# Performance work log

Hardware: AMD Instinct MI355X
Metric: run time of the kernel (lower is better)

Reference implementation:

```python
import jax, jax.numpy as jnp
import numpy as np

H = 16
D_MODEL = 1024
D_K = D_MODEL // H
L = 4096


def setup_inputs() -> dict:
    key = jax.random.key(0)
    ks = jax.random.split(key, 11)
    s = 1.0 / np.sqrt(D_MODEL)
    inp = {
        "query": jax.random.normal(ks[0], (L, D_MODEL), dtype=jnp.float32),
        "key": jax.random.normal(ks[1], (L, D_MODEL), dtype=jnp.float32),
        "value": jax.random.normal(ks[2], (L, D_MODEL), dtype=jnp.float32),
        "Wq": jax.random.uniform(ks[3], (D_MODEL, D_MODEL), jnp.float32, -s, s),
        "Wk": jax.random.uniform(ks[4], (D_MODEL, D_MODEL), jnp.float32, -s, s),
        "Wv": jax.random.uniform(ks[5], (D_MODEL, D_MODEL), jnp.float32, -s, s),
        "Wo": jax.random.uniform(ks[6], (D_MODEL, D_MODEL), jnp.float32, -s, s),
        "bq": jax.random.uniform(ks[7], (D_MODEL,), jnp.float32, -s, s),
        "bk": jax.random.uniform(ks[8], (D_MODEL,), jnp.float32, -s, s),
        "bv": jax.random.uniform(ks[9], (D_MODEL,), jnp.float32, -s, s),
        "bo": jax.random.uniform(ks[10], (D_MODEL,), jnp.float32, -s, s),
    }
    return inp


def reference(query, key, value, Wq, Wk, Wv, Wo, bq, bk, bv, bo):
    # projections: torch Linear computes x @ W.T + b
    def proj(x, W, b):
        # [L, d_model] -> [h, L, d_k]
        y = x @ W.T + b
        return y.reshape(L, H, D_K).transpose(1, 0, 2)

    q = proj(query, Wq, bq)   # [h, L, d_k]
    k = proj(key, Wk, bk)
    v = proj(value, Wv, bv)

    scores = jnp.einsum("hqd,hkd->hqk", q, k) / jnp.sqrt(jnp.float32(D_K))  # [h, L, L]
    p = jax.nn.softmax(scores, axis=-1)
    x = jnp.einsum("hqk,hkd->hqd", p, v)         # [h, L, d_k]
    x = x.transpose(1, 0, 2).reshape(L, H * D_K)  # [L, d_model]
    return x @ Wo.T + bo
```

## Files before the change

### kernel.cpp

```cpp
#include <hip/hip_runtime.h>

#define L_SEQ 4096
#define DM 1024
#define NH 16
#define DK 64

typedef short s16x8 __attribute__((ext_vector_type(8)));
typedef float f32x4 __attribute__((ext_vector_type(4)));
typedef float f32x8 __attribute__((ext_vector_type(8)));
typedef float f32x16 __attribute__((ext_vector_type(16)));
typedef unsigned u32x2 __attribute__((ext_vector_type(2)));
typedef unsigned short u16t;
typedef unsigned int u32t;

typedef __attribute__((address_space(1))) unsigned int as1_u32;
typedef __attribute__((address_space(3))) unsigned int as3_u32;

#define GLOAD_LDS16(gsrc, ldst) \
  __builtin_amdgcn_global_load_lds((as1_u32*)(gsrc), (as3_u32*)(ldst), 16, 0, 0)

__device__ __forceinline__ u16t f2bf(float f) {
  union { float f; unsigned u; } v; v.f = f;
  unsigned u = v.u;
  u += 0x7fffu + ((u >> 16) & 1u);
  return (u16t)(u >> 16);
}

__device__ __forceinline__ float fexp2(float x) {
  float r;
  asm("v_exp_f32 %0, %1" : "=v"(r) : "v"(x));
  return r;
}

__device__ __forceinline__ float bflo(u32t u) {
  union { u32t u; float f; } v; v.u = u << 16; return v.f;
}
__device__ __forceinline__ float bfhi(u32t u) {
  union { u32t u; float f; } v; v.u = u & 0xffff0000u; return v.f;
}

struct CvtArgs { const float* s[7]; u16t* d[7]; };

__global__ __launch_bounds__(256) void cvt_all(CvtArgs a) {
  int g = blockIdx.x * 256 + threadIdx.x;
  int seg, off;
  if (g < 1572864) { seg = g >> 19;               off = g & 524287; }
  else             { int t = g - 1572864; seg = 3 + (t >> 17); off = t & 131071; }
  const float* src = a.s[seg] + (size_t)off * 8;
  u16t* dst = a.d[seg] + (size_t)off * 8;
  float4 x = *(const float4*)(src);
  float4 y = *(const float4*)(src + 4);
  uint4 o;
  o.x = (u32t)f2bf(x.x) | ((u32t)f2bf(x.y) << 16);
  o.y = (u32t)f2bf(x.z) | ((u32t)f2bf(x.w) << 16);
  o.z = (u32t)f2bf(y.x) | ((u32t)f2bf(y.y) << 16);
  o.w = (u32t)f2bf(y.z) | ((u32t)f2bf(y.w) << 16);
  *(uint4*)dst = o;
}

struct QkvArgs {
  const u16t* A[3]; const u16t* Bm[3]; const float* bias[3]; u16t* C[3];
  float scale0;
};

__global__ __launch_bounds__(256)
void gemm_qkv(QkvArgs ga) {
  __shared__ unsigned char lds[2][2][8192];
  const int bid = blockIdx.x;
  const int z = bid >> 8;
  const int b = bid & 255;
  const int bc = (z == 2) ? (b & 31) : (b & 7);
  const int br = (z == 2) ? (b >> 5) : (b >> 3);
  const int N  = (z == 2) ? L_SEQ : DM;
  const float osc = (z == 0) ? ga.scale0 : 1.0f;
  const bool rowb = (z == 2);
  const u16t* A = ga.A[z];
  const u16t* Bm = ga.Bm[z];
  const float* bias = ga.bias[z];
  u16t* C = ga.C[z];
  const int K = DM;

  const int tid = threadIdx.x;
  const int lane = tid & 63;
  const int wv = tid >> 6;
  const int wr = wv >> 1, wc = wv & 1;
  const int l15 = lane & 15, l4 = lane >> 4;

  const int r_st = tid >> 2;
  const int c_st = (tid & 3) ^ ((r_st >> 1) & 3);
  const u16t* a0 = A + (size_t)(br * 128 + r_st) * K + c_st * 8;
  const u16t* a1 = a0 + (size_t)64 * K;
  const u16t* b0 = Bm + (size_t)(bc * 128 + r_st) * K + c_st * 8;
  const u16t* b1 = b0 + (size_t)64 * K;
  const int woff = wv * 1024;

  f32x4 acc[4][4] = {};

  auto stage = [&](int buf, int k0) {
    GLOAD_LDS16(a0 + k0, &lds[buf][0][woff]);
    GLOAD_LDS16(a1 + k0, &lds[buf][0][4096 + woff]);
    GLOAD_LDS16(b0 + k0, &lds[buf][1][woff]);
    GLOAD_LDS16(b1 + k0, &lds[buf][1][4096 + woff]);
  };

  const int nt = K >> 5;
  stage(0, 0);
  int buf = 0;
  for (int t = 0; t < nt; ++t) {
    __syncthreads();
    if (t + 1 < nt) stage(buf ^ 1, (t + 1) * 32);
    s16x8 af[4], bfr[4];
    #pragma unroll
    for (int m = 0; m < 4; ++m) {
      int r = wr * 64 + m * 16 + l15;
      int sl = l4 ^ ((r >> 1) & 3);
      af[m] = *(const s16x8*)&lds[buf][0][r * 64 + (sl << 4)];
    }
    #pragma unroll
    for (int n = 0; n < 4; ++n) {
      int r = wc * 64 + n * 16 + l15;
      int sl = l4 ^ ((r >> 1) & 3);
      bfr[n] = *(const s16x8*)&lds[buf][1][r * 64 + (sl << 4)];
    }
    #pragma unroll
    for (int m = 0; m < 4; ++m)
      #pragma unroll
      for (int n = 0; n < 4; ++n)
        acc[m][n] = __builtin_amdgcn_mfma_f32_16x16x32_bf16(af[m], bfr[n], acc[m][n], 0, 0, 0);
    buf ^= 1;
  }

  #pragma unroll
  for (int m = 0; m < 4; ++m) {
    #pragma unroll
    for (int n = 0; n < 4; ++n) {
      #pragma unroll
      for (int i = 0; i < 4; ++i) {
        int row = br * 128 + wr * 64 + m * 16 + l4 * 4 + i;
        int col = bc * 128 + wc * 64 + n * 16 + l15;
        float v = (acc[m][n][i] + (rowb ? bias[row] : bias[col])) * osc;
        C[(size_t)row * N + col] = f2bf(v);
      }
    }
  }
}

__global__ __launch_bounds__(256)
void gemm_out(const u16t* __restrict__ A, const u16t* __restrict__ B,
              const float* __restrict__ bias, float* __restrict__ C,
              int M, int N, int K) {
  __shared__ unsigned char lds[2][12288];
  const int tid = threadIdx.x;
  const int lane = tid & 63;
  const int wv = tid >> 6;
  const int wr = wv >> 1, wc = wv & 1;
  const int l15 = lane & 15, l4 = lane >> 4;
  const int bc = blockIdx.x, br = blockIdx.y;

  const int r_st = tid >> 2;
  const int c_st = (tid & 3) ^ ((r_st >> 1) & 3);
  const u16t* a0 = A + (size_t)(br * 128 + r_st) * K + c_st * 8;
  const u16t* a1 = a0 + (size_t)64 * K;
  const u16t* b0 = B + (size_t)(bc * 64 + r_st) * K + c_st * 8;
  const int woff = wv * 1024;

  f32x4 acc[4][2] = {};

  auto stage = [&](int buf, int k0) {
    GLOAD_LDS16(a0 + k0, &lds[buf][woff]);
    GLOAD_LDS16(a1 + k0, &lds[buf][4096 + woff]);
    GLOAD_LDS16(b0 + k0, &lds[buf][8192 + woff]);
  };

  const int nt = K >> 5;
  stage(0, 0);
  int buf = 0;
  for (int t = 0; t < nt; ++t) {
    __syncthreads();
    if (t + 1 < nt) stage(buf ^ 1, (t + 1) * 32);
    s16x8 af[4], bfr[2];
    #pragma unroll
    for (int m = 0; m < 4; ++m) {
      int r = wr * 64 + m * 16 + l15;
      int sl = l4 ^ ((r >> 1) & 3);
      af[m] = *(const s16x8*)&lds[buf][r * 64 + (sl << 4)];
    }
    #pragma unroll
    for (int n = 0; n < 2; ++n) {
      int r = wc * 32 + n * 16 + l15;
      int sl = l4 ^ ((r >> 1) & 3);
      bfr[n] = *(const s16x8*)&lds[buf][8192 + r * 64 + (sl << 4)];
    }
    #pragma unroll
    for (int m = 0; m < 4; ++m)
      #pragma unroll
      for (int n = 0; n < 2; ++n)
        acc[m][n] = __builtin_amdgcn_mfma_f32_16x16x32_bf16(af[m], bfr[n], acc[m][n], 0, 0, 0);
    buf ^= 1;
  }

  #pragma unroll
  for (int m = 0; m < 4; ++m) {
    #pragma unroll
    for (int n = 0; n < 2; ++n) {
      #pragma unroll
      for (int i = 0; i < 4; ++i) {
        int row = br * 128 + wr * 64 + m * 16 + l4 * 4 + i;
        int col = bc * 64 + wc * 32 + n * 16 + l15;
        C[(size_t)row * N + col] = acc[m][n][i] + bias[col];
      }
    }
  }
}

#define PKBF(dst, a, b) \
  asm("v_cvt_pk_bf16_f32 %0, %1, %2" : "=v"(dst) : "v"(a), "v"(b))

#define MAKE_FRAG(S, B, FR) { \
    u32t w0, w1, w2, w3; \
    PKBF(w0, S[B + 0], S[B + 1]); PKBF(w1, S[B + 2], S[B + 3]); \
    PKBF(w2, S[B + 4], S[B + 5]); PKBF(w3, S[B + 6], S[B + 7]); \
    u32x2 r02 = __builtin_amdgcn_permlane32_swap(w0, w2, false, false); \
    u32x2 r13 = __builtin_amdgcn_permlane32_swap(w1, w3, false, false); \
    union { u32t u[4]; s16x8 v; } uu; \
    uu.u[0] = r02[0]; uu.u[1] = r13[0]; uu.u[2] = r02[1]; uu.u[3] = r13[1]; \
    FR = uu.v; }

__global__ __launch_bounds__(512, 4)
void attn_fused(const u16t* __restrict__ Qp, const u16t* __restrict__ Kp,
                const u16t* __restrict__ VpT, u16t* __restrict__ Op0,
                u16t* __restrict__ Op1, float2* __restrict__ Ml0,
                float2* __restrict__ Ml1) {
  __shared__ unsigned char sStage[3][16384];

  const int tid = threadIdx.x;
  const int lane = tid & 63;
  const int w = tid >> 6;
  const int l31 = lane & 31;
  const int hi = lane >> 5;
  const int h = blockIdx.y;
  const int z = blockIdx.z;
  const int kvbase = z * (L_SEQ / 2);
  const int qrow = blockIdx.x * 256 + w * 32 + l31;
  u16t* Opz = z ? Op1 : Op0;
  float2* Mlz = z ? Ml1 : Ml0;

  s16x8 qf[4];
  {
    const u16t* qsrc = Qp + (size_t)qrow * DM + h * DK + hi * 8;
    #pragma unroll
    for (int c = 0; c < 4; ++c) qf[c] = *(const s16x8*)(qsrc + c * 16);
  }

  f32x16 acc0 = {}, acc1 = {};
  float lrow = 0.f;

  const u16t* kptr = Kp + (size_t)(kvbase + lane) * DM + h * DK + w * 8;
  const u16t* vptr = VpT + (size_t)(h * DK + lane) * L_SEQ + kvbase + w * 8;
  const int woffK = w * 1024;

  auto stage = [&](int buf) {
    GLOAD_LDS16(kptr, &sStage[buf][woffK]);
    GLOAD_LDS16(vptr, &sStage[buf][8192 + woffK]);
    kptr += 64 * DM;
    vptr += 64;
  };

  const int rdoff = (hi << 10) + (l31 << 4);

  auto compute = [&](const unsigned char* sb) {
    f32x16 st0 = {}, st1 = {};
    __builtin_amdgcn_s_setprio(1);
    #pragma unroll
    for (int c = 0; c < 4; ++c) {
      s16x8 kf0 = *(const s16x8*)(sb + c * 2048);
      s16x8 kf1 = *(const s16x8*)(sb + c * 2048 + 512);
      st0 = __builtin_amdgcn_mfma_f32_32x32x16_bf16(kf0, qf[c], st0, 0, 0, 0);
      st1 = __builtin_amdgcn_mfma_f32_32x32x16_bf16(kf1, qf[c], st1, 0, 0, 0);
    }
    __builtin_amdgcn_s_setprio(0);

    #pragma unroll
    for (int r = 0; r < 16; ++r) {
      st0[r] = fexp2(st0[r]);
      st1[r] = fexp2(st1[r]);
    }
    f32x16 sv = st0 + st1;
    f32x8 s8v = __builtin_shufflevector(sv, sv, 0, 1, 2, 3, 4, 5, 6, 7) +
                __builtin_shufflevector(sv, sv, 8, 9, 10, 11, 12, 13, 14, 15);
    f32x4 s4v = __builtin_shufflevector(s8v, s8v, 0, 1, 2, 3) +
                __builtin_shufflevector(s8v, s8v, 4, 5, 6, 7);
    float rs = (s4v[0] + s4v[1]) + (s4v[2] + s4v[3]);
    rs += __shfl_xor(rs, 32);
    lrow += rs;

    __builtin_amdgcn_s_setprio(1);
    #pragma unroll
    for (int cc = 0; cc < 4; ++cc) {
      s16x8 pfr;
      if (cc == 0)      MAKE_FRAG(st0, 0, pfr)
      else if (cc == 1) MAKE_FRAG(st0, 8, pfr)
      else if (cc == 2) MAKE_FRAG(st1, 0, pfr)
      else              MAKE_FRAG(st1, 8, pfr)
      s16x8 vf0 = *(const s16x8*)(sb + 8192 + cc * 2048);
      s16x8 vf1 = *(const s16x8*)(sb + 8192 + cc * 2048 + 512);
      acc0 = __builtin_amdgcn_mfma_f32_32x32x16_bf16(vf0, pfr, acc0, 0, 0, 0);
      acc1 = __builtin_amdgcn_mfma_f32_32x32x16_bf16(vf1, pfr, acc1, 0, 0, 0);
    }
    __builtin_amdgcn_s_setprio(0);
  };

  auto phase = [&](int bc, int bs) {
    asm volatile("s_waitcnt vmcnt(2)" ::: "memory");
    __builtin_amdgcn_s_barrier();
    __builtin_amdgcn_sched_barrier(0);
    stage(bs);
    compute(sStage[bc] + rdoff);
  };

  stage(0);
  stage(1);
  #pragma unroll 1
  for (int c = 0; c < 10; ++c) {
    phase(0, 2);
    phase(1, 0);
    phase(2, 1);
  }
  asm volatile("s_waitcnt vmcnt(2)" ::: "memory");
  __builtin_amdgcn_s_barrier();
  __builtin_amdgcn_sched_barrier(0);
  compute(sStage[0] + rdoff);
  asm volatile("s_waitcnt vmcnt(0)" ::: "memory");
  __builtin_amdgcn_s_barrier();
  __builtin_amdgcn_sched_barrier(0);
  compute(sStage[1] + rdoff);

  u16t* orow = Opz + (size_t)qrow * DM + h * DK;
  #pragma unroll
  for (int rq = 0; rq < 4; ++rq) {
    union { u16t h4[4]; uint2 v; } p0, p1;
    #pragma unroll
    for (int i = 0; i < 4; ++i) {
      p0.h4[i] = f2bf(acc0[4 * rq + i]);
      p1.h4[i] = f2bf(acc1[4 * rq + i]);
    }
    int d0 = 8 * rq + 4 * hi;
    *(uint2*)(orow + d0)      = p0.v;
    *(uint2*)(orow + 32 + d0) = p1.v;
  }
  if (hi == 0) Mlz[h * L_SEQ + qrow] = make_float2(0.f, lrow);
}

__global__ __launch_bounds__(256)
void attn_combine(const u16t* __restrict__ O0, const u16t* __restrict__ O1,
                  const float2* __restrict__ Ml0, const float2* __restrict__ Ml1,
                  u16t* __restrict__ AO) {
  int g = blockIdx.x * 256 + threadIdx.x;
  int qh = g >> 2;
  int d0 = (g & 3) * 16;
  int q = qh >> 4, h = qh & 15;
  size_t off = (size_t)q * DM + h * DK + d0;

  float2 ml0 = Ml0[h * L_SEQ + q];
  float2 ml1 = Ml1[h * L_SEQ + q];
  float m = fmaxf(ml0.x, ml1.x);
  float w0 = fexp2(ml0.x - m), w1 = fexp2(ml1.x - m);
  float inv = 1.0f / (ml0.y * w0 + ml1.y * w1);
  float s0 = w0 * inv, s1 = w1 * inv;

  uint4 a[2], b[2], o[2];
  a[0] = *(const uint4*)(O0 + off);     a[1] = *(const uint4*)(O0 + off + 8);
  b[0] = *(const uint4*)(O1 + off);     b[1] = *(const uint4*)(O1 + off + 8);
  #pragma unroll
  for (int k = 0; k < 2; ++k) {
    u32t* au = (u32t*)&a[k]; u32t* bu = (u32t*)&b[k]; u32t* ou = (u32t*)&o[k];
    #pragma unroll
    for (int j = 0; j < 4; ++j) {
      float lo = bflo(au[j]) * s0 + bflo(bu[j]) * s1;
      float hf = bfhi(au[j]) * s0 + bfhi(bu[j]) * s1;
      ou[j] = (u32t)f2bf(lo) | ((u32t)f2bf(hf) << 16);
    }
  }
  *(uint4*)(AO + off)     = o[0];
  *(uint4*)(AO + off + 8) = o[1];
}

extern "C" void kernel_launch(void* const* d_in, const int* in_sizes, int n_in,
                              void* d_out, int out_size, void* d_ws, size_t ws_size,
                              hipStream_t stream) {
  const float* query = (const float*)d_in[0];
  const float* key_  = (const float*)d_in[1];
  const float* value = (const float*)d_in[2];
  const float* Wq = (const float*)d_in[3];
  const float* Wk = (const float*)d_in[4];
  const float* Wv = (const float*)d_in[5];
  const float* Wo = (const float*)d_in[6];
  const float* bq = (const float*)d_in[7];
  const float* bk = (const float*)d_in[8];
  const float* bv = (const float*)d_in[9];
  const float* bo = (const float*)d_in[10];

  char* ws = (char*)d_ws;
  const size_t MB = 1u << 20;
  u16t* qb  = (u16t*)(ws + 0 * MB);
  u16t* kb  = (u16t*)(ws + 8 * MB);
  u16t* vb  = (u16t*)(ws + 16 * MB);
  u16t* wqb = (u16t*)(ws + 24 * MB);
  u16t* wkb = (u16t*)(ws + 26 * MB);
  u16t* wvb = (u16t*)(ws + 28 * MB);
  u16t* wob = (u16t*)(ws + 30 * MB);
  u16t* Qp  = (u16t*)(ws + 32 * MB);
  u16t* Kp  = (u16t*)(ws + 40 * MB);
  u16t* VpT = (u16t*)(ws + 48 * MB);
  u16t* AO  = (u16t*)(ws + 56 * MB);

  u16t* Op0   = (u16t*)(ws + 0 * MB);
  u16t* Op1   = (u16t*)(ws + 8 * MB);
  float2* Ml0 = (float2*)(ws + 16 * MB);
  float2* Ml1 = (float2*)(ws + 17 * MB);

  const float QSCALE = 0.125f * 1.4426950408889634f;

  CvtArgs ca;
  ca.s[0] = query; ca.s[1] = key_; ca.s[2] = value;
  ca.s[3] = Wq; ca.s[4] = Wk; ca.s[5] = Wv; ca.s[6] = Wo;
  ca.d[0] = qb; ca.d[1] = kb; ca.d[2] = vb;
  ca.d[3] = wqb; ca.d[4] = wkb; ca.d[5] = wvb; ca.d[6] = wob;
  cvt_all<<<dim3(8192), dim3(256), 0, stream>>>(ca);

  QkvArgs ga;
  ga.A[0] = qb;  ga.Bm[0] = wqb; ga.bias[0] = bq; ga.C[0] = Qp;
  ga.A[1] = kb;  ga.Bm[1] = wkb; ga.bias[1] = bk; ga.C[1] = Kp;
  ga.A[2] = wvb; ga.Bm[2] = vb;  ga.bias[2] = bv; ga.C[2] = VpT;
  ga.scale0 = QSCALE;
  gemm_qkv<<<dim3(768), dim3(256), 0, stream>>>(ga);

  attn_fused<<<dim3(L_SEQ / 256, NH, 2), dim3(512), 0, stream>>>(
      Qp, Kp, VpT, Op0, Op1, Ml0, Ml1);

  attn_combine<<<dim3(1024), dim3(256), 0, stream>>>(Op0, Op1, Ml0, Ml1, AO);

  gemm_out<<<dim3(DM / 64, L_SEQ / 128), dim3(256), 0, stream>>>(
      AO, wob, bo, (float*)d_out, L_SEQ, DM, DM);
}
```

Before: 155.5 us.

## Switch attention KV pipeline to double-buffered 128-key stages with two barriers

```diff
diff --git a/kernel.cpp b/kernel.cpp
--- a/kernel.cpp
+++ b/kernel.cpp
@@ -231,7 +231,7 @@
                 const u16t* __restrict__ VpT, u16t* __restrict__ Op0,
                 u16t* __restrict__ Op1, float2* __restrict__ Ml0,
                 float2* __restrict__ Ml1) {
-  __shared__ unsigned char sStage[3][16384];
+  __shared__ unsigned char sStage[2][32768];
 
   const int tid = threadIdx.x;
   const int lane = tid & 63;
@@ -256,25 +256,30 @@
   float lrow = 0.f;
 
   const u16t* kptr = Kp + (size_t)(kvbase + lane) * DM + h * DK + w * 8;
-  const u16t* vptr = VpT + (size_t)(h * DK + lane) * L_SEQ + kvbase + w * 8;
-  const int woffK = w * 1024;
+  const u16t* vptr = VpT + (size_t)(h * DK + lane) * L_SEQ + kvbase + w * 16;
+  const int kdst = w * 2048;
+  const int vdst = 16384 + 2 * w * 1024;
 
   auto stage = [&](int buf) {
-    GLOAD_LDS16(kptr, &sStage[buf][woffK]);
-    GLOAD_LDS16(vptr, &sStage[buf][8192 + woffK]);
-    kptr += 64 * DM;
-    vptr += 64;
+    GLOAD_LDS16(kptr,           &sStage[buf][kdst]);
+    GLOAD_LDS16(kptr + 64 * DM, &sStage[buf][kdst + 1024]);
+    GLOAD_LDS16(vptr,           &sStage[buf][vdst]);
+    GLOAD_LDS16(vptr + 8,       &sStage[buf][vdst + 1024]);
+    kptr += 128 * DM;
+    vptr += 128;
   };
 
-  const int rdoff = (hi << 10) + (l31 << 4);
-
-  auto compute = [&](const unsigned char* sb) {
+  const int rdK = (hi << 11) + (l31 << 4);
+  const int rdV = (hi << 10) + (l31 << 4);
+
+  auto compute = [&](const unsigned char* sb, int s) {
+    const unsigned char* sk = sb + (s << 10) + rdK;
     f32x16 st0 = {}, st1 = {};
     __builtin_amdgcn_s_setprio(1);
     #pragma unroll
     for (int c = 0; c < 4; ++c) {
-      s16x8 kf0 = *(const s16x8*)(sb + c * 2048);
-      s16x8 kf1 = *(const s16x8*)(sb + c * 2048 + 512);
+      s16x8 kf0 = *(const s16x8*)(sk + c * 4096);
+      s16x8 kf1 = *(const s16x8*)(sk + c * 4096 + 512);
       st0 = __builtin_amdgcn_mfma_f32_32x32x16_bf16(kf0, qf[c], st0, 0, 0, 0);
       st1 = __builtin_amdgcn_mfma_f32_32x32x16_bf16(kf1, qf[c], st1, 0, 0, 0);
     }
@@ -294,6 +299,7 @@
     rs += __shfl_xor(rs, 32);
     lrow += rs;
 
+    const unsigned char* svp = sb + 16384 + (s << 13) + rdV;
     __builtin_amdgcn_s_setprio(1);
     #pragma unroll
     for (int cc = 0; cc < 4; ++cc) {
@@ -302,38 +308,31 @@
       else if (cc == 1) MAKE_FRAG(st0, 8, pfr)
       else if (cc == 2) MAKE_FRAG(st1, 0, pfr)
       else              MAKE_FRAG(st1, 8, pfr)
-      s16x8 vf0 = *(const s16x8*)(sb + 8192 + cc * 2048);
-      s16x8 vf1 = *(const s16x8*)(sb + 8192 + cc * 2048 + 512);
+      s16x8 vf0 = *(const s16x8*)(svp + cc * 2048);
+      s16x8 vf1 = *(const s16x8*)(svp + cc * 2048 + 512);
       acc0 = __builtin_amdgcn_mfma_f32_32x32x16_bf16(vf0, pfr, acc0, 0, 0, 0);
       acc1 = __builtin_amdgcn_mfma_f32_32x32x16_bf16(vf1, pfr, acc1, 0, 0, 0);
     }
     __builtin_amdgcn_s_setprio(0);
   };
 
-  auto phase = [&](int bc, int bs) {
-    asm volatile("s_waitcnt vmcnt(2)" ::: "memory");
+  stage(0);
+  int buf = 0;
+  #pragma unroll 1
+  for (int p = 0; p < 16; ++p) {
+    __builtin_amdgcn_s_barrier();
+    if (p < 15) {
+      stage(buf ^ 1);
+      asm volatile("s_waitcnt vmcnt(4)" ::: "memory");
+    } else {
+      asm volatile("s_waitcnt vmcnt(0)" ::: "memory");
+    }
     __builtin_amdgcn_s_barrier();
     __builtin_amdgcn_sched_barrier(0);
-    stage(bs);
-    compute(sStage[bc] + rdoff);
-  };
-
-  stage(0);
-  stage(1);
-  #pragma unroll 1
-  for (int c = 0; c < 10; ++c) {
-    phase(0, 2);
-    phase(1, 0);
-    phase(2, 1);
-  }
-  asm volatile("s_waitcnt vmcnt(2)" ::: "memory");
-  __builtin_amdgcn_s_barrier();
-  __builtin_amdgcn_sched_barrier(0);
-  compute(sStage[0] + rdoff);
-  asm volatile("s_waitcnt vmcnt(0)" ::: "memory");
-  __builtin_amdgcn_s_barrier();
-  __builtin_amdgcn_sched_barrier(0);
-  compute(sStage[1] + rdoff);
+    compute(sStage[buf], 0);
+    compute(sStage[buf], 1);
+    buf ^= 1;
+  }
 
   u16t* orow = Opz + (size_t)qrow * DM + h * DK;
   #pragma unroll
```

After: 160.6 us. 3.3% more time.

## Software-pipeline QK^T of next tile with PV of previous tile in attention loop

Applied to the files above, without the earlier changes.

```diff
diff --git a/kernel.cpp b/kernel.cpp
--- a/kernel.cpp
+++ b/kernel.cpp
@@ -231,7 +231,7 @@
                 const u16t* __restrict__ VpT, u16t* __restrict__ Op0,
                 u16t* __restrict__ Op1, float2* __restrict__ Ml0,
                 float2* __restrict__ Ml1) {
-  __shared__ unsigned char sStage[3][16384];
+  __shared__ unsigned char sStage[4][16384];
 
   const int tid = threadIdx.x;
   const int lane = tid & 63;
@@ -268,8 +268,12 @@
 
   const int rdoff = (hi << 10) + (l31 << 4);
 
-  auto compute = [&](const unsigned char* sb) {
-    f32x16 st0 = {}, st1 = {};
+  f32x16 st0, st1;
+  s16x8 pfr[4];
+
+  auto qkt = [&](const unsigned char* sb) {
+    st0 = f32x16{};
+    st1 = f32x16{};
     __builtin_amdgcn_s_setprio(1);
     #pragma unroll
     for (int c = 0; c < 4; ++c) {
@@ -279,7 +283,21 @@
       st1 = __builtin_amdgcn_mfma_f32_32x32x16_bf16(kf1, qf[c], st1, 0, 0, 0);
     }
     __builtin_amdgcn_s_setprio(0);
-
+  };
+
+  auto pv = [&](const unsigned char* sb) {
+    __builtin_amdgcn_s_setprio(1);
+    #pragma unroll
+    for (int cc = 0; cc < 4; ++cc) {
+      s16x8 vf0 = *(const s16x8*)(sb + 8192 + cc * 2048);
+      s16x8 vf1 = *(const s16x8*)(sb + 8192 + cc * 2048 + 512);
+      acc0 = __builtin_amdgcn_mfma_f32_32x32x16_bf16(vf0, pfr[cc], acc0, 0, 0, 0);
+      acc1 = __builtin_amdgcn_mfma_f32_32x32x16_bf16(vf1, pfr[cc], acc1, 0, 0, 0);
+    }
+    __builtin_amdgcn_s_setprio(0);
+  };
+
+  auto softmax = [&]() {
     #pragma unroll
     for (int r = 0; r < 16; ++r) {
       st0[r] = fexp2(st0[r]);
@@ -293,47 +311,39 @@
     float rs = (s4v[0] + s4v[1]) + (s4v[2] + s4v[3]);
     rs += __shfl_xor(rs, 32);
     lrow += rs;
-
-    __builtin_amdgcn_s_setprio(1);
-    #pragma unroll
-    for (int cc = 0; cc < 4; ++cc) {
-      s16x8 pfr;
-      if (cc == 0)      MAKE_FRAG(st0, 0, pfr)
-      else if (cc == 1) MAKE_FRAG(st0, 8, pfr)
-      else if (cc == 2) MAKE_FRAG(st1, 0, pfr)
-      else              MAKE_FRAG(st1, 8, pfr)
-      s16x8 vf0 = *(const s16x8*)(sb + 8192 + cc * 2048);
-      s16x8 vf1 = *(const s16x8*)(sb + 8192 + cc * 2048 + 512);
-      acc0 = __builtin_amdgcn_mfma_f32_32x32x16_bf16(vf0, pfr, acc0, 0, 0, 0);
-      acc1 = __builtin_amdgcn_mfma_f32_32x32x16_bf16(vf1, pfr, acc1, 0, 0, 0);
-    }
-    __builtin_amdgcn_s_setprio(0);
-  };
-
-  auto phase = [&](int bc, int bs) {
+    MAKE_FRAG(st0, 0, pfr[0]);
+    MAKE_FRAG(st0, 8, pfr[1]);
+    MAKE_FRAG(st1, 0, pfr[2]);
+    MAKE_FRAG(st1, 8, pfr[3]);
+  };
+
+  stage(0);
+  stage(1);
+  asm volatile("s_waitcnt vmcnt(2)" ::: "memory");
+  __builtin_amdgcn_s_barrier();
+  __builtin_amdgcn_sched_barrier(0);
+  stage(2);
+  qkt(sStage[0] + rdoff);
+  softmax();
+
+  #pragma unroll 1
+  for (int t = 1; t <= 30; ++t) {
     asm volatile("s_waitcnt vmcnt(2)" ::: "memory");
     __builtin_amdgcn_s_barrier();
     __builtin_amdgcn_sched_barrier(0);
-    stage(bs);
-    compute(sStage[bc] + rdoff);
-  };
-
-  stage(0);
-  stage(1);
-  #pragma unroll 1
-  for (int c = 0; c < 10; ++c) {
-    phase(0, 2);
-    phase(1, 0);
-    phase(2, 1);
-  }
-  asm volatile("s_waitcnt vmcnt(2)" ::: "memory");
-  __builtin_amdgcn_s_barrier();
-  __builtin_amdgcn_sched_barrier(0);
-  compute(sStage[0] + rdoff);
+    if (t <= 29) stage((t + 2) & 3);
+    qkt(sStage[t & 3] + rdoff);
+    pv(sStage[(t - 1) & 3] + rdoff);
+    softmax();
+  }
+
   asm volatile("s_waitcnt vmcnt(0)" ::: "memory");
   __builtin_amdgcn_s_barrier();
   __builtin_amdgcn_sched_barrier(0);
-  compute(sStage[1] + rdoff);
+  qkt(sStage[3] + rdoff);
+  pv(sStage[2] + rdoff);
+  softmax();
+  pv(sStage[3] + rdoff);
 
   u16t* orow = Opz + (size_t)qrow * DM + h * DK;
   #pragma unroll
```

Result: no change. 158.0 us (+1.6%).
